# Performance work log

Measured on AMD Instinct MI355X. Metric: run time of the kernel, lower is better.

## Reference

```python
import jax, jax.numpy as jnp
import numpy as np

PI = np.pi


def ramp_filter(x):
    """skimage-style ramp filter along the detector axis (axis=2).
    x: [B, C, D, A] sinogram."""
    D = x.shape[2]
    P = max(64, int(2 ** np.ceil(np.log2(2 * D))))  # padded FFT size
    xp = jnp.pad(x, ((0, 0), (0, 0), (0, P - D), (0, 0)))
    # real-space ramp kernel (Kak & Slaney), then FFT -> frequency filter
    n = np.concatenate([np.arange(1, P // 2 + 1, 2), np.arange(P // 2 - 1, 0, -2)])
    f = np.zeros(P, dtype=np.float64)
    f[0] = 0.25
    f[1::2] = -1.0 / (PI * n) ** 2
    fourier_filter = jnp.asarray(2.0 * np.real(np.fft.fft(f)), dtype=jnp.float32)  # [P]
    proj = jnp.fft.fft(xp, axis=2) * fourier_filter[None, None, :, None]
    return jnp.real(jnp.fft.ifft(proj, axis=2))[:, :, :D, :].astype(x.dtype)


def setup_inputs() -> dict:
    key = jax.random.key(0)
    x = jax.random.normal(key, (2, 1, 512, 180), dtype=jnp.float32)  # [B,C,D,A]
    return {"x": x}


def reference(x):
    B, C, D, A = x.shape
    S = D  # circle=True -> in_size == out_size == detector count
    xf = ramp_filter(x)

    lin = jnp.arange(S, dtype=jnp.float32) * 2.0 / (S - 1) - 1.0
    xg = lin[None, :]  # [1,S], varies along columns (image x)
    yg = lin[:, None]  # [S,1], varies along rows  (image y)
    theta = jnp.deg2rad(jnp.arange(A, dtype=jnp.float32))

    # detector coordinate for each (angle, pixel): T = x*cos(th) - y*sin(th), in [-1,1]
    T = xg[None] * jnp.cos(theta)[:, None, None] - yg[None] * jnp.sin(theta)[:, None, None]  # [A,S,S]

    # grid X selects column i_theta exactly (align_corners=True semantics);
    # grid_sample thus reduces to 1-D linear interpolation along the detector axis.
    pix = (T + 1.0) * (D - 1) * 0.5  # pixel coords in [0, D-1] domain
    i0 = jnp.floor(pix)
    w1 = pix - i0
    i0 = i0.astype(jnp.int32)
    i1 = i0 + 1

    xt = jnp.transpose(xf, (0, 1, 3, 2))  # [B,C,A,D]
    a_idx = jnp.arange(A)[:, None, None]  # [A,1,1]

    def gather(idx):
        valid = ((idx >= 0) & (idx <= D - 1)).astype(xf.dtype)  # zero padding
        idxc = jnp.clip(idx, 0, D - 1)
        g = xt[:, :, a_idx, idxc]  # [B,C,A,S,S]
        return g * valid

    contrib = gather(i0) * (1.0 - w1) + gather(i1) * w1  # [B,C,A,S,S]
    reco = jnp.sum(contrib, axis=2)  # [B,C,S,S]

    circle_mask = ((xg ** 2 + yg ** 2) <= 1.0).astype(reco.dtype)  # [S,S]
    reco = reco * circle_mask
    return reco * jnp.float32(PI / (2.0 * A))
```

## Files before the change

kernel.cpp:

```cpp
#include <hip/hip_runtime.h>
#include <hip/hip_fp16.h>
#include <math.h>

#define D_DET 512
#define N_ANG 180
#define S_IMG 512
#define NPIX  (S_IMG * S_IMG)
#define T_MAX 63
#define WIN   32

typedef _Float16 half2v __attribute__((ext_vector_type(2)));

__device__ __constant__ float kPI = 3.14159265358979323846f;

__device__ __forceinline__ half2v pack_w1(float w) {
    return __builtin_bit_cast(half2v, __builtin_amdgcn_cvt_pkrtz(1.0f, w));
}

__global__ __launch_bounds__(512) void ramp_filter_kernel(
    const float* __restrict__ x, unsigned* __restrict__ xfh) {
    __shared__ float rp[4][640];
    __shared__ float xf[4][D_DET + 1];

    const int blk = blockIdx.x;
    const int bc  = blk / 45;
    const int a0  = (blk % 45) * 4;
    const int d   = threadIdx.x;

    float4 q = *(const float4*)(x + (bc * D_DET + d) * N_ANG + a0);
    rp[0][64 + d] = q.x;
    rp[1][64 + d] = q.y;
    rp[2][64 + d] = q.z;
    rp[3][64 + d] = q.w;
    if (d < 64) {
        #pragma unroll
        for (int r = 0; r < 4; ++r) { rp[r][d] = 0.0f; rp[r][576 + d] = 0.0f; }
    }
    if (d < 4) xf[d][D_DET] = 0.0f;
    __syncthreads();

    constexpr float PI_ = 3.14159265358979323846f;
    #pragma unroll
    for (int r = 0; r < 4; ++r) {
        const float* rm = &rp[r][64 + d];
        float acc = 0.5f * rm[0];
        #pragma unroll
        for (int k = 0; k < (T_MAX + 1) / 2; ++k) {
            const int   t = 2 * k + 1;
            const float h = -2.0f / (PI_ * PI_ * (float)(t * t));
            acc = fmaf(rm[-t] + rm[t], h, acc);
        }
        xf[r][d] = acc;
    }
    __syncthreads();

    #pragma unroll
    for (int r = 0; r < 4; ++r) {
        const float f0 = xf[r][d];
        const float dl = xf[r][d + 1] - f0;
        const unsigned lo = __half_as_ushort(__float2half_rn(f0));
        const unsigned hi = __half_as_ushort(__float2half_rn(dl));
        xfh[((a0 + r) * D_DET + d) * 2 + bc] = (hi << 16) | lo;
    }
}

__global__ __launch_bounds__(512) void backproj_kernel(
    const uint2* __restrict__ xfh, float* __restrict__ out) {
    __shared__ float4 trig4[N_ANG];
    __shared__ uint2  win[90 * WIN];
    __shared__ float2 red[256];

    const int tid = threadIdx.x;
    const int bi  = blockIdx.x >> 5;
    const int bj  = blockIdx.x & 31;
    const int i0  = bi << 4;
    const int j0  = bj << 4;

    if (tid < N_ANG) {
        float th = (float)tid * (kPI / 180.0f);
        float s, c;
        sincosf(th, &s, &c);
        float c5 = c * 255.5f, s5 = s * 255.5f;
        float bias = 255.5f, dmf = 0.0f;
        if (tid >= 90) {
            float x0 = (float)j0 * (2.0f / 511.0f) - 1.0f;
            float x1 = (float)(j0 + 15) * (2.0f / 511.0f) - 1.0f;
            float y0 = (float)i0 * (2.0f / 511.0f) - 1.0f;
            float y1 = (float)(i0 + 15) * (2.0f / 511.0f) - 1.0f;
            float pmin = 255.5f + fminf(c5 * x0, c5 * x1)
                                + fminf(-s5 * y0, -s5 * y1);
            int dmin = (int)floorf(pmin) - 1;
            dmin = dmin < 0 ? 0 : (dmin > (D_DET - WIN) ? (D_DET - WIN) : dmin);
            dmin &= ~1;
            bias = 255.5f - (float)dmin;
            dmf  = (float)dmin;
        }
        trig4[tid] = make_float4(c5, s5, bias, dmf);
    }
    __syncthreads();

    {
        const uint4* __restrict__ src4 = (const uint4*)xfh;
        uint4* win4 = (uint4*)win;
        #pragma unroll
        for (int f = tid; f < 90 * (WIN / 2); f += 512) {
            int a    = f >> 4;
            int e    = f & 15;
            int ag   = 90 + a;
            int dmin = (int)trig4[ag].w;
            win4[f]  = src4[((ag << 9) + dmin) >> 1];
            win4[f]  = src4[(((ag << 9) + dmin) >> 1) + e];
        }
    }
    __syncthreads();

    const int half = tid >> 8;
    const int sub  = (tid >> 6) & 3;
    const int lane = tid & 63;
    const int px   = tid & 255;
    const int i = i0 + ((sub >> 1) << 3) + (lane >> 3);
    const int j = j0 + ((sub & 1) << 3) + (lane & 7);

    const float xP = (float)j * (2.0f / 511.0f) - 1.0f;
    const float yP = (float)i * (2.0f / 511.0f) - 1.0f;
    const float m  = xP * xP + yP * yP;
    const bool inc = (m <= 1.0f);
    const float xS = inc ? xP : 0.0f;
    const float yS = inc ? yP : 0.0f;

    float a0 = 0.0f, a1 = 0.0f;
    if (__any(inc)) {
        if (half == 0) {
            #pragma unroll 6
            for (int a = 0; a < 90; ++a) {
                float4 t  = trig4[a];
                float pc  = fmaf(xS, t.x, fmaf(yS, -t.y, 255.5f));
                pc        = fmaxf(pc, 0.0f);
                int   fi  = (int)pc;
                float w   = __builtin_amdgcn_fractf(pc);
                half2v hw = pack_w1(w);
                uint2  g  = xfh[(a << 9) + fi];
                a0 = __builtin_amdgcn_fdot2(hw, __builtin_bit_cast(half2v, g.x), a0, false);
                a1 = __builtin_amdgcn_fdot2(hw, __builtin_bit_cast(half2v, g.y), a1, false);
            }
        } else {
            #pragma unroll 6
            for (int a = 90; a < N_ANG; ++a) {
                float4 t  = trig4[a];
                float pc  = fmaf(xS, t.x, fmaf(yS, -t.y, t.z));
                pc        = fminf(fmaxf(pc, 0.0f), (float)(WIN - 1));
                int   fi  = (int)pc;
                float w   = __builtin_amdgcn_fractf(pc);
                half2v hw = pack_w1(w);
                uint2  g  = win[((a - 90) << 5) + fi];
                a0 = __builtin_amdgcn_fdot2(hw, __builtin_bit_cast(half2v, g.x), a0, false);
                a1 = __builtin_amdgcn_fdot2(hw, __builtin_bit_cast(half2v, g.y), a1, false);
            }
        }
    }

    if (half == 1) red[px] = make_float2(a0, a1);
    __syncthreads();
    if (half == 0) {
        const float2 r = red[px];
        const float msk = inc ? (kPI / (2.0f * (float)N_ANG)) : 0.0f;
        const int p = i * S_IMG + j;
        out[p]        = (a0 + r.x) * msk;
        out[NPIX + p] = (a1 + r.y) * msk;
    }
}

extern "C" void kernel_launch(void* const* d_in, const int* in_sizes, int n_in,
                              void* d_out, int out_size, void* d_ws, size_t ws_size,
                              hipStream_t stream) {
    const float* x   = (const float*)d_in[0];
    float*       out = (float*)d_out;
    unsigned*    xfh = (unsigned*)d_ws;

    ramp_filter_kernel<<<90, 512, 0, stream>>>(x, xfh);
    backproj_kernel<<<1024, 512, 0, stream>>>((const uint2*)xfh, out);
}
```

Measured before the change: 27.18 us.

## Rebalance angle split and replace trig table with incremental rotation recurrence

Moves the angle split between the two half-blocks from 90/90 to 72/108, so more angles go through the shared-memory window path and fewer through the global-gather path. It also drops the per-angle trig table and instead computes detector coordinates by rotating (p,q) by one degree each step, reseeding with sincos every 36 angles. A redundant duplicate window load is removed. The aim is to cut LDS traffic and global gathers, but the recurrence accumulates float rounding error, and the two halves may now do unequal amounts of work.

New measurement: 29.87 us. +9.9%, slower.

```diff
diff --git a/kernel.cpp b/kernel.cpp
--- a/kernel.cpp
+++ b/kernel.cpp
@@ -7,7 +7,11 @@
 #define S_IMG 512
 #define NPIX  (S_IMG * S_IMG)
 #define T_MAX 63
+#define AG    72
+#define AL    108
 #define WIN   32
+#define CD    0.99984769515639124f
+#define SD    0.01745240643728351f
 
 typedef _Float16 half2v __attribute__((ext_vector_type(2)));
 
@@ -66,8 +70,9 @@
 
 __global__ __launch_bounds__(512) void backproj_kernel(
     const uint2* __restrict__ xfh, float* __restrict__ out) {
-    __shared__ float4 trig4[N_ANG];
-    __shared__ uint2  win[90 * WIN];
+    __shared__ float  dminF[AL];
+    __shared__ int    dminI[AL];
+    __shared__ uint2  win[AL * WIN];
     __shared__ float2 red[256];
 
     const int tid = threadIdx.x;
@@ -76,40 +81,33 @@
     const int i0  = bi << 4;
     const int j0  = bj << 4;
 
-    if (tid < N_ANG) {
-        float th = (float)tid * (kPI / 180.0f);
+    if (tid < AL) {
+        float th = (float)(AG + tid) * (kPI / 180.0f);
         float s, c;
         sincosf(th, &s, &c);
         float c5 = c * 255.5f, s5 = s * 255.5f;
-        float bias = 255.5f, dmf = 0.0f;
-        if (tid >= 90) {
-            float x0 = (float)j0 * (2.0f / 511.0f) - 1.0f;
-            float x1 = (float)(j0 + 15) * (2.0f / 511.0f) - 1.0f;
-            float y0 = (float)i0 * (2.0f / 511.0f) - 1.0f;
-            float y1 = (float)(i0 + 15) * (2.0f / 511.0f) - 1.0f;
-            float pmin = 255.5f + fminf(c5 * x0, c5 * x1)
-                                + fminf(-s5 * y0, -s5 * y1);
-            int dmin = (int)floorf(pmin) - 1;
-            dmin = dmin < 0 ? 0 : (dmin > (D_DET - WIN) ? (D_DET - WIN) : dmin);
-            dmin &= ~1;
-            bias = 255.5f - (float)dmin;
-            dmf  = (float)dmin;
-        }
-        trig4[tid] = make_float4(c5, s5, bias, dmf);
+        float x0 = (float)j0 * (2.0f / 511.0f) - 1.0f;
+        float x1 = (float)(j0 + 15) * (2.0f / 511.0f) - 1.0f;
+        float y0 = (float)i0 * (2.0f / 511.0f) - 1.0f;
+        float y1 = (float)(i0 + 15) * (2.0f / 511.0f) - 1.0f;
+        float pmin = 255.5f + fminf(c5 * x0, c5 * x1)
+                            + fminf(-s5 * y0, -s5 * y1);
+        int dmin = (int)floorf(pmin) - 1;
+        dmin = dmin < 0 ? 0 : (dmin > (D_DET - WIN) ? (D_DET - WIN) : dmin);
+        dmin &= ~1;
+        dminI[tid] = dmin;
+        dminF[tid] = 255.5f - (float)dmin;
     }
     __syncthreads();
 
     {
         const uint4* __restrict__ src4 = (const uint4*)xfh;
         uint4* win4 = (uint4*)win;
-        #pragma unroll
-        for (int f = tid; f < 90 * (WIN / 2); f += 512) {
+        for (int f = tid; f < AL * (WIN / 2); f += 512) {
             int a    = f >> 4;
             int e    = f & 15;
-            int ag   = 90 + a;
-            int dmin = (int)trig4[ag].w;
-            win4[f]  = src4[((ag << 9) + dmin) >> 1];
-            win4[f]  = src4[(((ag << 9) + dmin) >> 1) + e];
+            int dmin = dminI[a];
+            win4[f]  = src4[((((AG + a) << 9) + dmin) >> 1) + e];
         }
     }
     __syncthreads();
@@ -131,30 +129,58 @@
     float a0 = 0.0f, a1 = 0.0f;
     if (__any(inc)) {
         if (half == 0) {
-            #pragma unroll 6
-            for (int a = 0; a < 90; ++a) {
-                float4 t  = trig4[a];
-                float pc  = fmaf(xS, t.x, fmaf(yS, -t.y, 255.5f));
-                pc        = fmaxf(pc, 0.0f);
-                int   fi  = (int)pc;
-                float w   = __builtin_amdgcn_fractf(pc);
-                half2v hw = pack_w1(w);
-                uint2  g  = xfh[(a << 9) + fi];
-                a0 = __builtin_amdgcn_fdot2(hw, __builtin_bit_cast(half2v, g.x), a0, false);
-                a1 = __builtin_amdgcn_fdot2(hw, __builtin_bit_cast(half2v, g.y), a1, false);
+            #pragma unroll 1
+            for (int c = 0; c < AG / 36; ++c) {
+                const int abase = c * 36;
+                float th = (float)abase * (kPI / 180.0f);
+                float sn, cs;
+                sincosf(th, &sn, &cs);
+                float p = xS * (cs * 255.5f) - yS * (sn * 255.5f);
+                float q = xS * (sn * 255.5f) + yS * (cs * 255.5f);
+                #pragma unroll 6
+                for (int k = 0; k < 36; ++k) {
+                    float pc  = fmaxf(p + 255.5f, 0.0f);
+                    int   fi  = (int)pc;
+                    float w   = __builtin_amdgcn_fractf(pc);
+                    half2v hw = pack_w1(w);
+                    uint2  g  = xfh[((abase + k) << 9) + fi];
+                    a0 = __builtin_amdgcn_fdot2(hw, __builtin_bit_cast(half2v, g.x), a0, false);
+                    a1 = __builtin_amdgcn_fdot2(hw, __builtin_bit_cast(half2v, g.y), a1, false);
+                    float pn = fmaf(CD, p, -SD * q);
+                    q        = fmaf(CD, q,  SD * p);
+                    p = pn;
+                }
             }
         } else {
-            #pragma unroll 6
-            for (int a = 90; a < N_ANG; ++a) {
-                float4 t  = trig4[a];
-                float pc  = fmaf(xS, t.x, fmaf(yS, -t.y, t.z));
-                pc        = fminf(fmaxf(pc, 0.0f), (float)(WIN - 1));
-                int   fi  = (int)pc;
-                float w   = __builtin_amdgcn_fractf(pc);
-                half2v hw = pack_w1(w);
-                uint2  g  = win[((a - 90) << 5) + fi];
-                a0 = __builtin_amdgcn_fdot2(hw, __builtin_bit_cast(half2v, g.x), a0, false);
-                a1 = __builtin_amdgcn_fdot2(hw, __builtin_bit_cast(half2v, g.y), a1, false);
+            const float4* __restrict__ bias4 = (const float4*)dminF;
+            #pragma unroll 1
+            for (int c = 0; c < AL / 36; ++c) {
+                const int abase = c * 36;
+                float th = (float)(AG + abase) * (kPI / 180.0f);
+                float sn, cs;
+                sincosf(th, &sn, &cs);
+                float p = xS * (cs * 255.5f) - yS * (sn * 255.5f);
+                float q = xS * (sn * 255.5f) + yS * (cs * 255.5f);
+                #pragma unroll 3
+                for (int gq = 0; gq < 9; ++gq) {
+                    const float4 bs = bias4[c * 9 + gq];
+                    #pragma unroll
+                    for (int jj = 0; jj < 4; ++jj) {
+                        const int al = abase + gq * 4 + jj;
+                        const float bias = (jj == 0) ? bs.x : (jj == 1) ? bs.y
+                                         : (jj == 2) ? bs.z : bs.w;
+                        float pcW = fminf(fmaxf(p + bias, 0.0f), (float)(WIN - 1));
+                        int   fi  = (int)pcW;
+                        float w   = __builtin_amdgcn_fractf(pcW);
+                        half2v hw = pack_w1(w);
+                        uint2  g  = win[(al << 5) + fi];
+                        a0 = __builtin_amdgcn_fdot2(hw, __builtin_bit_cast(half2v, g.x), a0, false);
+                        a1 = __builtin_amdgcn_fdot2(hw, __builtin_bit_cast(half2v, g.y), a1, false);
+                        float pn = fmaf(CD, p, -SD * q);
+                        q        = fmaf(CD, q,  SD * p);
+                        p = pn;
+                    }
+                }
             }
         }
     }
```
